# Performance work log

Measured on AMD Instinct MI355X. Metric: run time of the kernel, lower is better.

Reference implementation:

```python
import jax, jax.numpy as jnp
import numpy as np

N = 131072   # query points
K = 32       # top-k gaussians per point
G = 100000   # num_gaussians
DELTA = 0.05
EPS = 1e-8


def setup_inputs() -> dict:
    key = jax.random.key(0)
    ks = jax.random.split(key, 7)
    coords = jax.random.normal(ks[0], (N, 3), jnp.float32) * 2.0
    # PSF covariance: symmetric PSD per point (A A^T + 0.1 I)
    A = jax.random.normal(ks[1], (N, 3, 3), jnp.float32) * 0.3
    Sigma_psf = jnp.einsum('nij,nkj->nik', A, A) + 0.1 * jnp.eye(3, dtype=jnp.float32)
    mu = jax.random.normal(ks[2], (G, 3), jnp.float32) * 2.0
    scaling = jax.random.uniform(ks[3], (G, 3), jnp.float32, minval=0.5, maxval=1.5)
    rotation_g = jax.random.normal(ks[4], (G, 4), jnp.float32)
    color = jax.random.uniform(ks[5], (G,), jnp.float32)
    top_k_idcs = jax.random.randint(ks[6], (N, K), 0, G)
    return {"coords": coords, "Sigma_psf": Sigma_psf, "mu": mu, "scaling": scaling,
            "rotation_g": rotation_g, "color": color, "top_k_idcs": top_k_idcs}


def _quat_to_rot(q):
    # q: (G,4) wxyz -> R: (G,3,3), matches fused kernel math (rsqrt normalize)
    inv_norm = jax.lax.rsqrt(jnp.sum(q * q, axis=-1, keepdims=True) + EPS)
    qn = q * inv_norm
    w, x, y, z = qn[..., 0], qn[..., 1], qn[..., 2], qn[..., 3]
    x2, y2, z2 = x * x, y * y, z * z
    xy, xz, yz = x * y, x * z, y * z
    wx, wy, wz = w * x, w * y, w * z
    r0 = jnp.stack([1.0 - 2.0 * (y2 + z2), 2.0 * (xy - wz), 2.0 * (xz + wy)], axis=-1)
    r1 = jnp.stack([2.0 * (xy + wz), 1.0 - 2.0 * (x2 + z2), 2.0 * (yz - wx)], axis=-1)
    r2 = jnp.stack([2.0 * (xz - wy), 2.0 * (yz + wx), 1.0 - 2.0 * (x2 + y2)], axis=-1)
    return jnp.stack([r0, r1, r2], axis=-2)


def _compute_sigma(scaling, rotation_g, scale_scale):
    # Sigma = R diag(s^2) R^T, s = scaling * scale_scale
    R = _quat_to_rot(rotation_g)            # (G,3,3)
    M = R * (scaling * scale_scale)[:, None, :]  # scale columns
    return jnp.einsum('gik,gjk->gij', M, M)      # (G,3,3)


def _mahalanobis(sig, v):
    # sig: (N,K,3,3) symmetric; v: (N,K,3). Explicit 3x3 inverse, same as torch kernel.
    a = sig[..., 0, 0]; b = sig[..., 0, 1]; c = sig[..., 0, 2]
    e = sig[..., 1, 1]; f = sig[..., 1, 2]
    h = sig[..., 2, 1]; i = sig[..., 2, 2]
    det = a * (e * i - f * h) - b * (b * i - f * c) + c * (b * h - e * c)
    inv_det = 1.0 / (det + EPS)
    inv00 = (e * i - f * h) * inv_det
    inv01 = (c * h - b * i) * inv_det
    inv02 = (b * f - c * e) * inv_det
    inv11 = (a * i - c * c) * inv_det
    inv12 = (c * b - a * f) * inv_det
    inv22 = (a * e - b * b) * inv_det
    vx, vy, vz = v[..., 0], v[..., 1], v[..., 2]
    t0 = inv00 * vx + inv01 * vy + inv02 * vz
    t1 = inv01 * vx + inv11 * vy + inv12 * vz
    t2 = inv02 * vx + inv12 * vy + inv22 * vz
    return vx * t0 + vy * t1 + vz * t2


def reference(coords, Sigma_psf, mu, scaling, rotation_g, color, top_k_idcs):
    scale_scale = 1.0  # default; thresholding branch inactive
    mus = mu[top_k_idcs]                         # (N,K,3)
    x_minus_mu = coords[:, None, :] - mus        # (N,K,3)
    sigmas = _compute_sigma(scaling, rotation_g, scale_scale)[top_k_idcs]  # (N,K,3,3)
    sigmas = (sigmas + Sigma_psf[:, None, :, :]).astype(jnp.float32)
    inner = _mahalanobis(sigmas, x_minus_mu)     # (N,K)
    w = jnp.exp(-0.5 * inner)
    sum_w = jnp.sum(w, axis=1, keepdims=True)
    w_nrmd = w / (sum_w + DELTA)
    intensity = jnp.sum(w_nrmd * color[top_k_idcs], axis=1)  # (N,)
    return intensity
```

## Files before the change

### kernel.cpp

```cpp
#include <hip/hip_runtime.h>
#include <hip/hip_fp16.h>

#define DELTA 0.05f
#define EPS 1e-8f

union H2F { __half2 h; float f; };

__global__ __launch_bounds__(256) void precompute_gauss(
    const float* __restrict__ mu,
    const float* __restrict__ scaling,
    const float* __restrict__ rot,
    const float* __restrict__ color,
    float4* __restrict__ table, int G)
{
    int g = blockIdx.x * blockDim.x + threadIdx.x;
    if (g >= G) return;
    float qw = rot[g*4+0], qx = rot[g*4+1], qy = rot[g*4+2], qz = rot[g*4+3];
    float inv_norm = rsqrtf(qw*qw + qx*qx + qy*qy + qz*qz + EPS);
    qw *= inv_norm; qx *= inv_norm; qy *= inv_norm; qz *= inv_norm;
    float x2 = qx*qx, y2 = qy*qy, z2 = qz*qz;
    float xy = qx*qy, xz = qx*qz, yz = qy*qz;
    float wx = qw*qx, wy = qw*qy, wz = qw*qz;
    float R00 = 1.f - 2.f*(y2 + z2), R01 = 2.f*(xy - wz),       R02 = 2.f*(xz + wy);
    float R10 = 2.f*(xy + wz),       R11 = 1.f - 2.f*(x2 + z2), R12 = 2.f*(yz - wx);
    float R20 = 2.f*(xz - wy),       R21 = 2.f*(yz + wx),       R22 = 1.f - 2.f*(x2 + y2);
    float s0 = scaling[g*3+0], s1 = scaling[g*3+1], s2 = scaling[g*3+2];
    float d0 = s0*s0, d1 = s1*s1, d2 = s2*s2;
    float S00 = R00*R00*d0 + R01*R01*d1 + R02*R02*d2;
    float S01 = R00*R10*d0 + R01*R11*d1 + R02*R12*d2;
    float S02 = R00*R20*d0 + R01*R21*d1 + R02*R22*d2;
    float S11 = R10*R10*d0 + R11*R11*d1 + R12*R12*d2;
    float S12 = R10*R20*d0 + R11*R21*d1 + R12*R22*d2;
    float S22 = R20*R20*d0 + R21*R21*d1 + R22*R22*d2;

    H2F u01, u21, u22, uc;
    u01.h = __floats2half2_rn(S00, S01);
    u21.h = __floats2half2_rn(S02, S11);
    u22.h = __floats2half2_rn(S12, S22);
    uc.h  = __floats2half2_rn(color[g], 0.f);

    float mx = mu[g*3+0], my = mu[g*3+1], mz = mu[g*3+2];
    table[(size_t)g*2+0] = make_float4(mx, my, mz, u01.f);
    table[(size_t)g*2+1] = make_float4(u21.f, u22.f, uc.f, 0.f);
}

__global__ __launch_bounds__(256) void gsvr_dual(
    const float* __restrict__ coords,
    const float* __restrict__ psf,
    const int*   __restrict__ idcs,
    const float4* __restrict__ table,
    float* __restrict__ out, int n_pts)
{
    int tid    = blockIdx.x * blockDim.x + threadIdx.x;
    int waveId = tid >> 6;
    int lane   = tid & 63;
    int pA     = waveId * 2;
    if (pA >= n_pts) return;
    int pB     = min(pA + 1, n_pts - 1);
    int parity = lane & 1;
    int t      = lane >> 1;

    int gA = __builtin_nontemporal_load(idcs + (size_t)pA*32 + t);
    int gB = __builtin_nontemporal_load(idcs + (size_t)pB*32 + t);

    float4 vA = table[(size_t)gA*2 + parity];
    float4 vB = table[(size_t)gB*2 + parity];

    int pm = parity ? pB : pA;
    float cx = __builtin_nontemporal_load(coords + (size_t)pm*3+0);
    float cy = __builtin_nontemporal_load(coords + (size_t)pm*3+1);
    float cz = __builtin_nontemporal_load(coords + (size_t)pm*3+2);
    const float* sp = psf + (size_t)pm*9;
    float pa = __builtin_nontemporal_load(sp+0);
    float pb = __builtin_nontemporal_load(sp+1);
    float pc = __builtin_nontemporal_load(sp+2);
    float pe = __builtin_nontemporal_load(sp+4);
    float pf = __builtin_nontemporal_load(sp+5);
    float pi = __builtin_nontemporal_load(sp+8);

    float4 oA, oB;
    oA.x = __shfl_xor(vA.x, 1); oA.y = __shfl_xor(vA.y, 1);
    oA.z = __shfl_xor(vA.z, 1); oA.w = __shfl_xor(vA.w, 1);
    oB.x = __shfl_xor(vB.x, 1); oB.y = __shfl_xor(vB.y, 1);
    oB.z = __shfl_xor(vB.z, 1); oB.w = __shfl_xor(vB.w, 1);
    float4 r0 = parity ? oB : vA;
    float4 r1 = parity ? vB : oA;

    H2F u01, u21, u22, uc;
    u01.f = r0.w; u21.f = r1.x; u22.f = r1.y; uc.f = r1.z;
    float2 s01 = __half22float2(u01.h);
    float2 s21 = __half22float2(u21.h);
    float2 s22 = __half22float2(u22.h);
    float  col = __half22float2(uc.h).x;

    float a = s01.x + pa, b = s01.y + pb, c = s21.x + pc;
    float e = s21.y + pe, f = s22.x + pf, i = s22.y + pi;
    float vx = cx - r0.x, vy = cy - r0.y, vz = cz - r0.z;

    float ei_fh = e*i - f*f;
    float det = a*ei_fh - b*(b*i - f*c) + c*(b*f - e*c);
    float inv_det = 1.0f / (det + EPS);
    float i00 = ei_fh * inv_det;
    float i01 = (c*f - b*i) * inv_det;
    float i02 = (b*f - c*e) * inv_det;
    float i11 = (a*i - c*c) * inv_det;
    float i12 = (c*b - a*f) * inv_det;
    float i22 = (a*e - b*b) * inv_det;

    float q0 = i00*vx + i01*vy + i02*vz;
    float q1 = i01*vx + i11*vy + i12*vz;
    float q2 = i02*vx + i12*vy + i22*vz;
    float inner = vx*q0 + vy*q1 + vz*q2;

    float w  = __expf(-0.5f * inner);
    float wc = w * col;

    #pragma unroll
    for (int m = 32; m >= 2; m >>= 1) {
        w  += __shfl_xor(w,  m);
        wc += __shfl_xor(wc, m);
    }
    int po = pA + lane;
    if (lane < 2 && po < n_pts)
        __builtin_nontemporal_store(wc / (w + DELTA), out + po);
}

__global__ __launch_bounds__(256) void gsvr_fallback(
    const float* __restrict__ coords,
    const float* __restrict__ psf,
    const int*   __restrict__ idcs,
    const float* __restrict__ mu,
    const float* __restrict__ scaling,
    const float* __restrict__ rot,
    const float* __restrict__ color,
    float* __restrict__ out, int n_pts)
{
    int tid = blockIdx.x * blockDim.x + threadIdx.x;
    int p  = tid >> 5;
    int kk = tid & 31;
    if (p >= n_pts) return;

    float cx = coords[p*3+0], cy = coords[p*3+1], cz = coords[p*3+2];
    const float* sp = psf + (size_t)p*9;
    float pa = sp[0], pb = sp[1], pc = sp[2], pe = sp[4], pf = sp[5], pi = sp[8];

    int g = idcs[p*32 + kk];
    float qw = rot[g*4+0], qx = rot[g*4+1], qy = rot[g*4+2], qz = rot[g*4+3];
    float inv_norm = rsqrtf(qw*qw + qx*qx + qy*qy + qz*qz + EPS);
    qw *= inv_norm; qx *= inv_norm; qy *= inv_norm; qz *= inv_norm;
    float x2 = qx*qx, y2 = qy*qy, z2 = qz*qz;
    float xy = qx*qy, xz = qx*qz, yz = qy*qz;
    float wx = qw*qx, wy = qw*qy, wz = qw*qz;
    float R00 = 1.f - 2.f*(y2 + z2), R01 = 2.f*(xy - wz),       R02 = 2.f*(xz + wy);
    float R10 = 2.f*(xy + wz),       R11 = 1.f - 2.f*(x2 + z2), R12 = 2.f*(yz - wx);
    float R20 = 2.f*(xz - wy),       R21 = 2.f*(yz + wx),       R22 = 1.f - 2.f*(x2 + y2);
    float s0 = scaling[g*3+0], s1 = scaling[g*3+1], s2 = scaling[g*3+2];
    float dd0 = s0*s0, dd1 = s1*s1, dd2 = s2*s2;
    float S00 = R00*R00*dd0 + R01*R01*dd1 + R02*R02*dd2;
    float S01 = R00*R10*dd0 + R01*R11*dd1 + R02*R12*dd2;
    float S02 = R00*R20*dd0 + R01*R21*dd1 + R02*R22*dd2;
    float S11 = R10*R10*dd0 + R11*R11*dd1 + R12*R12*dd2;
    float S12 = R10*R20*dd0 + R11*R21*dd1 + R12*R22*dd2;
    float S22 = R20*R20*dd0 + R21*R21*dd1 + R22*R22*dd2;

    float a = S00 + pa, b = S01 + pb, c = S02 + pc;
    float e = S11 + pe, f = S12 + pf, i = S22 + pi;
    float vx = cx - mu[g*3+0], vy = cy - mu[g*3+1], vz = cz - mu[g*3+2];

    float ei_fh = e*i - f*f;
    float det = a*ei_fh - b*(b*i - f*c) + c*(b*f - e*c);
    float inv_det = 1.0f / (det + EPS);
    float i00 = ei_fh * inv_det;
    float i01 = (c*f - b*i) * inv_det;
    float i02 = (b*f - c*e) * inv_det;
    float i11 = (a*i - c*c) * inv_det;
    float i12 = (c*b - a*f) * inv_det;
    float i22 = (a*e - b*b) * inv_det;

    float q0 = i00*vx + i01*vy + i02*vz;
    float q1 = i01*vx + i11*vy + i12*vz;
    float q2 = i02*vx + i12*vy + i22*vz;
    float inner = vx*q0 + vy*q1 + vz*q2;

    float w  = __expf(-0.5f * inner);
    float wc = w * color[g];

    #pragma unroll
    for (int m = 16; m >= 1; m >>= 1) {
        w  += __shfl_xor(w,  m);
        wc += __shfl_xor(wc, m);
    }
    if (kk == 0) out[p] = wc / (w + DELTA);
}

extern "C" void kernel_launch(void* const* d_in, const int* in_sizes, int n_in,
                              void* d_out, int out_size, void* d_ws, size_t ws_size,
                              hipStream_t stream)
{
    const float* coords  = (const float*)d_in[0];
    const float* psf     = (const float*)d_in[1];
    const float* mu      = (const float*)d_in[2];
    const float* scaling = (const float*)d_in[3];
    const float* rot     = (const float*)d_in[4];
    const float* color   = (const float*)d_in[5];
    const int*   idcs    = (const int*)d_in[6];
    float* out = (float*)d_out;

    int n_pts = in_sizes[0] / 3;
    int G     = in_sizes[5];

    size_t need = (size_t)G * 8 * sizeof(float);

    if (ws_size >= need) {
        float4* table = (float4*)d_ws;
        precompute_gauss<<<(G + 255) / 256, 256, 0, stream>>>(mu, scaling, rot, color, table, G);
        long long waves   = ((long long)n_pts + 1) / 2;
        long long threads = waves * 64;
        gsvr_dual<<<(int)((threads + 255) / 256), 256, 0, stream>>>(
            coords, psf, idcs, table, out, n_pts);
    } else {
        int threads = n_pts * 32;
        gsvr_fallback<<<(threads + 255) / 256, 256, 0, stream>>>(
            coords, psf, idcs, mu, scaling, rot, color, out, n_pts);
    }
}
```

Measured before the change: 45.33 us.

## Convert gather kernel to persistent grid-stride loop with software-pipelined prefetch

Replaces the one-wave-per-point-pair kernel with a persistent kernel of 2048 blocks, where each wave loops over pairs with a stride of the total wave count. It prefetches indices two iterations ahead and the table entries, coords and PSF one iteration ahead, so the dependent index-to-table gather latency overlaps with compute on the current pair. Launch bounds now request 6 blocks per CU. The cost is more registers per thread and fewer concurrent waves than the original flat launch, which may reduce the latency hiding that occupancy provided before.

```diff
diff --git a/kernel.cpp b/kernel.cpp
--- a/kernel.cpp
+++ b/kernel.cpp
@@ -44,28 +44,72 @@
     table[(size_t)g*2+1] = make_float4(u21.f, u22.f, uc.f, 0.f);
 }
 
-__global__ __launch_bounds__(256) void gsvr_dual(
+__device__ __forceinline__ void task_wwc(
+    float4 vA, float4 vB, int parity,
+    float cx, float cy, float cz,
+    float pa, float pb, float pc, float pe, float pf, float pi,
+    float& w_out, float& wc_out)
+{
+    float4 oA, oB;
+    oA.x = __shfl_xor(vA.x, 1); oA.y = __shfl_xor(vA.y, 1);
+    oA.z = __shfl_xor(vA.z, 1); oA.w = __shfl_xor(vA.w, 1);
+    oB.x = __shfl_xor(vB.x, 1); oB.y = __shfl_xor(vB.y, 1);
+    oB.z = __shfl_xor(vB.z, 1); oB.w = __shfl_xor(vB.w, 1);
+    float4 r0 = parity ? oB : vA;
+    float4 r1 = parity ? vB : oA;
+
+    H2F u01, u21, u22, uc;
+    u01.f = r0.w; u21.f = r1.x; u22.f = r1.y; uc.f = r1.z;
+    float2 s01 = __half22float2(u01.h);
+    float2 s21 = __half22float2(u21.h);
+    float2 s22 = __half22float2(u22.h);
+    float  col = __half22float2(uc.h).x;
+
+    float a = s01.x + pa, b = s01.y + pb, c = s21.x + pc;
+    float e = s21.y + pe, f = s22.x + pf, i = s22.y + pi;
+    float vx = cx - r0.x, vy = cy - r0.y, vz = cz - r0.z;
+
+    float ei_fh = e*i - f*f;
+    float det = a*ei_fh - b*(b*i - f*c) + c*(b*f - e*c);
+    float inv_det = 1.0f / (det + EPS);
+    float i00 = ei_fh * inv_det;
+    float i01 = (c*f - b*i) * inv_det;
+    float i02 = (b*f - c*e) * inv_det;
+    float i11 = (a*i - c*c) * inv_det;
+    float i12 = (c*b - a*f) * inv_det;
+    float i22 = (a*e - b*b) * inv_det;
+
+    float q0 = i00*vx + i01*vy + i02*vz;
+    float q1 = i01*vx + i11*vy + i12*vz;
+    float q2 = i02*vx + i12*vy + i22*vz;
+    float inner = vx*q0 + vy*q1 + vz*q2;
+
+    float w = __expf(-0.5f * inner);
+    w_out  = w;
+    wc_out = w * col;
+}
+
+__global__ __launch_bounds__(256, 6) void gsvr_pipe(
     const float* __restrict__ coords,
     const float* __restrict__ psf,
     const int*   __restrict__ idcs,
     const float4* __restrict__ table,
-    float* __restrict__ out, int n_pts)
-{
-    int tid    = blockIdx.x * blockDim.x + threadIdx.x;
-    int waveId = tid >> 6;
-    int lane   = tid & 63;
-    int pA     = waveId * 2;
-    if (pA >= n_pts) return;
-    int pB     = min(pA + 1, n_pts - 1);
+    float* __restrict__ out, int n_pts, int n_pairs, int n_waves)
+{
+    int gtid   = blockIdx.x * blockDim.x + threadIdx.x;
+    int wid    = gtid >> 6;
+    int lane   = gtid & 63;
     int parity = lane & 1;
     int t      = lane >> 1;
-
+    if (wid >= n_pairs) return;
+
+    int k = wid;
+
+    int pA = 2*k, pB = min(2*k+1, n_pts-1);
     int gA = __builtin_nontemporal_load(idcs + (size_t)pA*32 + t);
     int gB = __builtin_nontemporal_load(idcs + (size_t)pB*32 + t);
-
     float4 vA = table[(size_t)gA*2 + parity];
     float4 vB = table[(size_t)gB*2 + parity];
-
     int pm = parity ? pB : pA;
     float cx = __builtin_nontemporal_load(coords + (size_t)pm*3+0);
     float cy = __builtin_nontemporal_load(coords + (size_t)pm*3+1);
@@ -78,51 +122,58 @@
     float pf = __builtin_nontemporal_load(sp+5);
     float pi = __builtin_nontemporal_load(sp+8);
 
-    float4 oA, oB;
-    oA.x = __shfl_xor(vA.x, 1); oA.y = __shfl_xor(vA.y, 1);
-    oA.z = __shfl_xor(vA.z, 1); oA.w = __shfl_xor(vA.w, 1);
-    oB.x = __shfl_xor(vB.x, 1); oB.y = __shfl_xor(vB.y, 1);
-    oB.z = __shfl_xor(vB.z, 1); oB.w = __shfl_xor(vB.w, 1);
-    float4 r0 = parity ? oB : vA;
-    float4 r1 = parity ? vB : oA;
-
-    H2F u01, u21, u22, uc;
-    u01.f = r0.w; u21.f = r1.x; u22.f = r1.y; uc.f = r1.z;
-    float2 s01 = __half22float2(u01.h);
-    float2 s21 = __half22float2(u21.h);
-    float2 s22 = __half22float2(u22.h);
-    float  col = __half22float2(uc.h).x;
-
-    float a = s01.x + pa, b = s01.y + pb, c = s21.x + pc;
-    float e = s21.y + pe, f = s22.x + pf, i = s22.y + pi;
-    float vx = cx - r0.x, vy = cy - r0.y, vz = cz - r0.z;
-
-    float ei_fh = e*i - f*f;
-    float det = a*ei_fh - b*(b*i - f*c) + c*(b*f - e*c);
-    float inv_det = 1.0f / (det + EPS);
-    float i00 = ei_fh * inv_det;
-    float i01 = (c*f - b*i) * inv_det;
-    float i02 = (b*f - c*e) * inv_det;
-    float i11 = (a*i - c*c) * inv_det;
-    float i12 = (c*b - a*f) * inv_det;
-    float i22 = (a*e - b*b) * inv_det;
-
-    float q0 = i00*vx + i01*vy + i02*vz;
-    float q1 = i01*vx + i11*vy + i12*vz;
-    float q2 = i02*vx + i12*vy + i22*vz;
-    float inner = vx*q0 + vy*q1 + vz*q2;
-
-    float w  = __expf(-0.5f * inner);
-    float wc = w * col;
-
-    #pragma unroll
-    for (int m = 32; m >= 2; m >>= 1) {
-        w  += __shfl_xor(w,  m);
-        wc += __shfl_xor(wc, m);
-    }
-    int po = pA + lane;
-    if (lane < 2 && po < n_pts)
-        __builtin_nontemporal_store(wc / (w + DELTA), out + po);
+    int kN = k + n_waves;
+    int gA_n = 0, gB_n = 0;
+    if (kN < n_pairs) {
+        gA_n = __builtin_nontemporal_load(idcs + (size_t)(2*kN)*32 + t);
+        gB_n = __builtin_nontemporal_load(idcs + (size_t)min(2*kN+1, n_pts-1)*32 + t);
+    }
+
+    for (;;) {
+        bool hasNext = (kN < n_pairs);
+        float4 vA2, vB2;
+        float cx2, cy2, cz2, pa2, pb2, pc2, pe2, pf2, pi2;
+        int gA_nn = 0, gB_nn = 0;
+        if (hasNext) {
+            vA2 = table[(size_t)gA_n*2 + parity];
+            vB2 = table[(size_t)gB_n*2 + parity];
+            int qA = 2*kN, qB = min(2*kN+1, n_pts-1);
+            int qm = parity ? qB : qA;
+            cx2 = __builtin_nontemporal_load(coords + (size_t)qm*3+0);
+            cy2 = __builtin_nontemporal_load(coords + (size_t)qm*3+1);
+            cz2 = __builtin_nontemporal_load(coords + (size_t)qm*3+2);
+            const float* sq = psf + (size_t)qm*9;
+            pa2 = __builtin_nontemporal_load(sq+0);
+            pb2 = __builtin_nontemporal_load(sq+1);
+            pc2 = __builtin_nontemporal_load(sq+2);
+            pe2 = __builtin_nontemporal_load(sq+4);
+            pf2 = __builtin_nontemporal_load(sq+5);
+            pi2 = __builtin_nontemporal_load(sq+8);
+            int kNN = kN + n_waves;
+            if (kNN < n_pairs) {
+                gA_nn = __builtin_nontemporal_load(idcs + (size_t)(2*kNN)*32 + t);
+                gB_nn = __builtin_nontemporal_load(idcs + (size_t)min(2*kNN+1, n_pts-1)*32 + t);
+            }
+        }
+
+        float w, wc;
+        task_wwc(vA, vB, parity, cx, cy, cz, pa, pb, pc, pe, pf, pi, w, wc);
+        #pragma unroll
+        for (int m = 32; m >= 2; m >>= 1) {
+            w  += __shfl_xor(w,  m);
+            wc += __shfl_xor(wc, m);
+        }
+        int po = 2*k + lane;
+        if (lane < 2 && po < n_pts)
+            __builtin_nontemporal_store(wc / (w + DELTA), out + po);
+
+        if (!hasNext) break;
+        vA = vA2; vB = vB2;
+        cx = cx2; cy = cy2; cz = cz2;
+        pa = pa2; pb = pb2; pc = pc2; pe = pe2; pf = pf2; pi = pi2;
+        gA_n = gA_nn; gB_n = gB_nn;
+        k = kN; kN = k + n_waves;
+    }
 }
 
 __global__ __launch_bounds__(256) void gsvr_fallback(
@@ -214,10 +265,12 @@
     if (ws_size >= need) {
         float4* table = (float4*)d_ws;
         precompute_gauss<<<(G + 255) / 256, 256, 0, stream>>>(mu, scaling, rot, color, table, G);
-        long long waves   = ((long long)n_pts + 1) / 2;
-        long long threads = waves * 64;
-        gsvr_dual<<<(int)((threads + 255) / 256), 256, 0, stream>>>(
-            coords, psf, idcs, table, out, n_pts);
+        int n_pairs = (n_pts + 1) / 2;
+        int blocks  = 2048;
+        int n_waves = blocks * (256 / 64);
+        if (n_waves > n_pairs) n_waves = n_pairs;
+        gsvr_pipe<<<blocks, 256, 0, stream>>>(
+            coords, psf, idcs, table, out, n_pts, n_pairs, n_waves);
     } else {
         int threads = n_pts * 32;
         gsvr_fallback<<<(threads + 255) / 256, 256, 0, stream>>>(
```

New measurement: 52.53 us. +15.9%, slower.
